# Kernel tuning notes

Measured on AMD Instinct MI355X. Metric: run time of the kernel, lower is better.

The kernel has to match this reference:

```python
import jax, jax.numpy as jnp
import numpy as np

B = 1024        # number of graphs in batch
NNODES = 64     # nodes per graph
NODE = 4        # node feature size
EDGEF = 2       # edge feature size
HID = 32        # hidden_dim
NFACT = 3       # num_factories
NE = 1024       # edges per graph (self.edges list length)


def setup_inputs() -> dict:
    key = jax.random.key(0)
    ks = jax.random.split(key, 12)
    rng = np.random.default_rng(1)
    # per-graph edge list (self.edges in the torch module)
    edges = rng.integers(0, NNODES, size=(NE, 2))
    edges_src = jnp.asarray(edges[:, 0], dtype=jnp.int32)   # [NE]
    edges_dst = jnp.asarray(edges[:, 1], dtype=jnp.int32)   # [NE]
    # batched edge_index for EdgeConv: same per-graph edges offset by b*NNODES
    offs = np.arange(B, dtype=np.int64)[:, None] * NNODES   # [B,1]
    ei_src = (edges[:, 0][None, :] + offs).reshape(-1)
    ei_dst = (edges[:, 1][None, :] + offs).reshape(-1)
    edge_index = jnp.asarray(np.stack([ei_src, ei_dst], 0), dtype=jnp.int32)  # [2, B*NE]

    N = B * NNODES
    E = B * NE
    x = jax.random.normal(ks[0], (N, NODE), dtype=jnp.float32)
    edge_attr = jax.random.normal(ks[1], (E, EDGEF), dtype=jnp.float32)
    action = jax.random.uniform(ks[2], (B, NE + NFACT), dtype=jnp.float32)

    s = 0.1
    W1 = jax.random.normal(ks[3], (2 * NODE + EDGEF, HID), dtype=jnp.float32) * s
    b1 = jnp.zeros((HID,), jnp.float32)
    W2 = jax.random.normal(ks[4], (HID, HID), dtype=jnp.float32) * s
    b2 = jnp.zeros((HID,), jnp.float32)
    D = (NODE + HID) * 2 + 1  # 73
    Wl = jax.random.normal(ks[5], (D, HID), dtype=jnp.float32) * s
    bl = jnp.zeros((HID,), jnp.float32)
    Wv = jax.random.normal(ks[6], (HID, 1), dtype=jnp.float32) * s
    bv = jnp.zeros((1,), jnp.float32)

    return {"x": x, "edge_index": edge_index, "edge_attr": edge_attr,
            "action": action, "edges_src": edges_src, "edges_dst": edges_dst,
            "W1": W1, "b1": b1, "W2": W2, "b2": b2,
            "Wl": Wl, "bl": bl, "Wv": Wv, "bv": bv}


def reference(x, edge_index, edge_attr, action, edges_src, edges_dst,
              W1, b1, W2, b2, Wl, bl, Wv, bv):
    N = x.shape[0]
    src = edge_index[0]  # flow='target_to_source': x_i = x[src], aggregate at src
    dst = edge_index[1]
    # EdgeConv message: MLP(cat[x_i, x_j, edge_attr])
    tmp = jnp.concatenate([x[src], x[dst], edge_attr], axis=1)  # [E, 10]
    msg = jax.nn.relu(tmp @ W1 + b1) @ W2 + b2                  # [E, HID]
    x_pp = jax.ops.segment_sum(msg, src, num_segments=N)        # scatter-add
    # concat node feats with conv output, split into graphs
    h = jnp.concatenate([x, x_pp], axis=1).reshape(B, NNODES, NODE + HID)  # [B,NN,36]
    # gather per-edge endpoint features
    ef = jnp.concatenate([h[:, edges_src], h[:, edges_dst]], axis=2)       # [B,NE,72]
    # factory features: last NFACT nodes duplicated
    pf = jnp.concatenate([h[:, -NFACT:], h[:, -NFACT:]], axis=-1)          # [B,NF,72]
    feats = jnp.concatenate([ef, pf], axis=1)                               # [B,NE+NF,72]
    concat = jnp.concatenate([feats, action[..., None]], axis=-1)           # [B,NE+NF,73]
    hidden = jax.nn.relu(concat @ Wl + bl)                                  # [B,NE+NF,HID]
    v = hidden @ Wv + bv                                                    # [B,NE+NF,1]
    return jnp.sum(v, axis=1).squeeze(-1)                                   # [B]
```

## Files before the change

kernel.cpp:

```cpp
#include <hip/hip_runtime.h>

#define NNODES 64
#define HID 32
#define NFACT 3
#define NE 1024
#define NROWS (NE + NFACT)
#define TPB 256
#define STR 36
#define QSTRH 20
#define MAXTILES 128
#define EPT (NE / TPB)

typedef short bf16x8 __attribute__((ext_vector_type(8)));
typedef float f32x4  __attribute__((ext_vector_type(4)));
typedef float f32x16 __attribute__((ext_vector_type(16)));

__device__ __forceinline__ unsigned pack_bf2(float lo, float hi) {
    unsigned ul = __builtin_bit_cast(unsigned, lo);
    unsigned uh = __builtin_bit_cast(unsigned, hi);
    ul += 0x7fffu + ((ul >> 16) & 1u);
    uh += 0x7fffu + ((uh >> 16) & 1u);
    return (ul >> 16) | (uh & 0xffff0000u);
}
__device__ __forceinline__ short f2bf(float f) {
    unsigned u = __builtin_bit_cast(unsigned, f);
    u += 0x7fffu + ((u >> 16) & 1u);
    return (short)(u >> 16);
}
__device__ __forceinline__ float bflo(unsigned u) { return __builtin_bit_cast(float, u << 16); }
__device__ __forceinline__ float bfhi(unsigned u) { return __builtin_bit_cast(float, u & 0xffff0000u); }
__device__ __forceinline__ float4 fma4(float a, float4 w, float4 c) {
    c.x = fmaf(a, w.x, c.x); c.y = fmaf(a, w.y, c.y);
    c.z = fmaf(a, w.z, c.z); c.w = fmaf(a, w.w, c.w);
    return c;
}

__global__ __launch_bounds__(TPB, 4) void critic_fused(
    const float* __restrict__ x,
    const float* __restrict__ edge_attr,
    const float* __restrict__ action,
    const int*   __restrict__ es,
    const int*   __restrict__ ed,
    const float* __restrict__ W1,
    const float* __restrict__ b1,
    const float* __restrict__ W2,
    const float* __restrict__ b2,
    const float* __restrict__ Wl,
    const float* __restrict__ bl,
    const float* __restrict__ Wv,
    const float* __restrict__ bv,
    float* __restrict__ out)
{
    const int b    = blockIdx.x;
    const int tid  = threadIdx.x;
    const int lane = tid & 63;
    const int wv   = tid >> 6;
    const int quad = lane >> 4;
    const int m16  = lane & 15;
    const int kh   = quad * 8;

    __shared__ __align__(16) float4 xs4[NNODES];
    __shared__ __align__(16) float  xpp[NNODES * STR];
    __shared__ __align__(16) float  qp0[NNODES * STR];
    __shared__ __align__(16) float  qp1[NNODES * STR];
    __shared__ __align__(16) float  W1s[10 * HID];
    __shared__ float  b1s[HID];
    __shared__ float  wred[TPB / 64];
    __shared__ int    sdeg[NNODES], soff[NNODES], scnt[NNODES];
    __shared__ int    tns[MAXTILES];
    __shared__ int    pep[MAXTILES * 16];
    __shared__ int    snt;

    unsigned* qh0 = (unsigned*)qp0;
    unsigned* qh1 = (unsigned*)qp1;

    if (tid < NNODES) { xs4[tid] = ((const float4*)x)[b * NNODES + tid]; sdeg[tid] = 0; scnt[tid] = 0; }
    if (tid < 80) ((float4*)W1s)[tid] = ((const float4*)W1)[tid];
    if (tid < HID) b1s[tid] = b1[tid];
    if (tid < MAXTILES) tns[tid] = 0;
#pragma unroll
    for (int i = 0; i < MAXTILES * 16 / TPB; i++) pep[tid + i * TPB] = 0xFFF;
#pragma unroll 1
    for (int i = tid; i < NNODES * STR; i += TPB) xpp[i] = 0.0f;

    int ces[EPT], ced[EPT];
#pragma unroll
    for (int i = 0; i < EPT; i++) {
        ces[i] = es[tid + i * TPB];
        ced[i] = ed[tid + i * TPB];
    }
    __syncthreads();

#pragma unroll
    for (int i = 0; i < EPT; i++) atomicAdd(&sdeg[ces[i]], 1);
    {
        const int n  = lane;
        const int k0 = wv * 8;
        const float4 xv = xs4[n];
        const float4* b1v = (const float4*)&b1s[k0];
        float4 q1a = b1v[0], q1b = b1v[1];
        float4 q2a = make_float4(0.f, 0.f, 0.f, 0.f), q2b = q2a;
#pragma unroll 1
        for (int i = 0; i < 4; i++) {
            const float xi = (i == 0) ? xv.x : (i == 1) ? xv.y : (i == 2) ? xv.z : xv.w;
            const float4* wa = (const float4*)&W1s[i * HID + k0];
            const float4* wb = (const float4*)&W1s[(4 + i) * HID + k0];
            q1a = fma4(xi, wa[0], q1a); q1b = fma4(xi, wa[1], q1b);
            q2a = fma4(xi, wb[0], q2a); q2b = fma4(xi, wb[1], q2b);
        }
        uint4 p1, p2;
        p1.x = pack_bf2(q1a.x, q1a.y); p1.y = pack_bf2(q1a.z, q1a.w);
        p1.z = pack_bf2(q1b.x, q1b.y); p1.w = pack_bf2(q1b.z, q1b.w);
        p2.x = pack_bf2(q2a.x, q2a.y); p2.y = pack_bf2(q2a.z, q2a.w);
        p2.z = pack_bf2(q2b.x, q2b.y); p2.w = pack_bf2(q2b.z, q2b.w);
        *(uint4*)&qh0[n * QSTRH + wv * 4] = p1;
        *(uint4*)&qh1[n * QSTRH + wv * 4] = p2;
    }
    __syncthreads();

    if (tid < NNODES) {
        const int cnt = (sdeg[tid] + 15) >> 4;
        int scan = cnt;
#pragma unroll
        for (int o = 1; o < 64; o <<= 1) {
            const int v = __shfl_up(scan, o);
            if (tid >= o) scan += v;
        }
        const int base = scan - cnt;
        soff[tid] = base;
        if (tid == NNODES - 1) snt = scan;
#pragma unroll 1
        for (int j = 0; j < cnt; j++) tns[base + j] = tid;
    }
    __syncthreads();

#pragma unroll
    for (int i = 0; i < EPT; i++) {
        const int n = ces[i];
        const int idx = atomicAdd(&scnt[n], 1);
        pep[soff[n] * 16 + idx] = (tid + i * TPB) | (ced[i] << 12) | (n << 18);
    }
    __syncthreads();

    {
        const float2* ea2 = (const float2*)edge_attr + (size_t)b * NE;
        const int NW   = TPB / 64;
        const int klo  = (lane >> 5) * 8;
        const int klo2 = klo >> 1;
        const int n32  = lane & 31;

        const float4* w8l = (const float4*)&W1s[8 * HID + klo];
        const float4* w8h = (const float4*)&W1s[8 * HID + 16 + klo];
        const float4* w9l = (const float4*)&W1s[9 * HID + klo];
        const float4* w9h = (const float4*)&W1s[9 * HID + 16 + klo];
        const float4 w8a = w8l[0], w8b = w8l[1], w8c = w8h[0], w8d = w8h[1];
        const float4 w9a = w9l[0], w9b = w9l[1], w9c = w9h[0], w9d = w9h[1];

        bf16x8 bfA, bfB;
#pragma unroll
        for (int j = 0; j < 8; j++) {
            bfA[j] = f2bf(W2[(klo + j) * HID + n32]);
            bfB[j] = f2bf(W2[(16 + klo + j) * HID + n32]);
        }

        const int np = (snt + 1) >> 1;

#pragma unroll 1
        for (int p = wv; p < np; p += NW) {
            const int raw = pep[p * 32 + n32];
            const int tA  = tns[2 * p];
            const int tB  = tns[2 * p + 1];
            const int e    = raw & 0xFFF;
            const bool pad = (e == 0xFFF);
            const int d0   = (raw >> 12) & 63;
            const int nd   = (raw >> 18) & 63;
            const float2 ea = ea2[pad ? 0 : e];

            const uint4 A1 = *(const uint4*)&qh0[nd * QSTRH + klo2];
            const uint4 A2 = *(const uint4*)&qh0[nd * QSTRH + 8 + klo2];
            const uint4 G1 = *(const uint4*)&qh1[d0 * QSTRH + klo2];
            const uint4 G2 = *(const uint4*)&qh1[d0 * QSTRH + 8 + klo2];

            const float hx0 = fmaxf(bflo(A1.x) + bflo(G1.x) + ea.x * w8a.x + ea.y * w9a.x, 0.f);
            const float hx1 = fmaxf(bfhi(A1.x) + bfhi(G1.x) + ea.x * w8a.y + ea.y * w9a.y, 0.f);
            const float hx2 = fmaxf(bflo(A1.y) + bflo(G1.y) + ea.x * w8a.z + ea.y * w9a.z, 0.f);
            const float hx3 = fmaxf(bfhi(A1.y) + bfhi(G1.y) + ea.x * w8a.w + ea.y * w9a.w, 0.f);
            const float hx4 = fmaxf(bflo(A1.z) + bflo(G1.z) + ea.x * w8b.x + ea.y * w9b.x, 0.f);
            const float hx5 = fmaxf(bfhi(A1.z) + bfhi(G1.z) + ea.x * w8b.y + ea.y * w9b.y, 0.f);
            const float hx6 = fmaxf(bflo(A1.w) + bflo(G1.w) + ea.x * w8b.z + ea.y * w9b.z, 0.f);
            const float hx7 = fmaxf(bfhi(A1.w) + bfhi(G1.w) + ea.x * w8b.w + ea.y * w9b.w, 0.f);
            const float hy0 = fmaxf(bflo(A2.x) + bflo(G2.x) + ea.x * w8c.x + ea.y * w9c.x, 0.f);
            const float hy1 = fmaxf(bfhi(A2.x) + bfhi(G2.x) + ea.x * w8c.y + ea.y * w9c.y, 0.f);
            const float hy2 = fmaxf(bflo(A2.y) + bflo(G2.y) + ea.x * w8c.z + ea.y * w9c.z, 0.f);
            const float hy3 = fmaxf(bfhi(A2.y) + bfhi(G2.y) + ea.x * w8c.w + ea.y * w9c.w, 0.f);
            const float hy4 = fmaxf(bflo(A2.z) + bflo(G2.z) + ea.x * w8d.x + ea.y * w9d.x, 0.f);
            const float hy5 = fmaxf(bfhi(A2.z) + bfhi(G2.z) + ea.x * w8d.y + ea.y * w9d.y, 0.f);
            const float hy6 = fmaxf(bflo(A2.w) + bflo(G2.w) + ea.x * w8d.z + ea.y * w9d.z, 0.f);
            const float hy7 = fmaxf(bfhi(A2.w) + bfhi(G2.w) + ea.x * w8d.w + ea.y * w9d.w, 0.f);

            uint4 pkA, pkB;
            pkA.x = pad ? 0u : pack_bf2(hx0, hx1);
            pkA.y = pad ? 0u : pack_bf2(hx2, hx3);
            pkA.z = pad ? 0u : pack_bf2(hx4, hx5);
            pkA.w = pad ? 0u : pack_bf2(hx6, hx7);
            pkB.x = pad ? 0u : pack_bf2(hy0, hy1);
            pkB.y = pad ? 0u : pack_bf2(hy2, hy3);
            pkB.z = pad ? 0u : pack_bf2(hy4, hy5);
            pkB.w = pad ? 0u : pack_bf2(hy6, hy7);
            const bf16x8 afA = __builtin_bit_cast(bf16x8, pkA);
            const bf16x8 afB = __builtin_bit_cast(bf16x8, pkB);

            f32x16 c;
#pragma unroll
            for (int j = 0; j < 16; j++) c[j] = 0.0f;
            c = __builtin_amdgcn_mfma_f32_32x32x16_bf16(afA, bfA, c, 0, 0, 0);
            c = __builtin_amdgcn_mfma_f32_32x32x16_bf16(afB, bfB, c, 0, 0, 0);

            float sA = ((c[0] + c[1]) + (c[2] + c[3])) + ((c[4] + c[5]) + (c[6] + c[7]));
            float sB = ((c[8] + c[9]) + (c[10] + c[11])) + ((c[12] + c[13]) + (c[14] + c[15]));
            sA += __shfl_xor(sA, 32);
            sB += __shfl_xor(sB, 32);
            const int   nst = (lane < 32) ? tA : tB;
            const float sv  = (lane < 32) ? sA : sB;
            atomicAdd(&xpp[nst * STR + n32], sv);
        }
    }
    __syncthreads();

    bf16x8 bP1a, bP1b, bP2a, bP2b;
#pragma unroll
    for (int j = 0; j < 8; j++) {
        bP1a[j] = f2bf(Wl[(4 + kh + j) * HID + m16]);
        bP1b[j] = f2bf(Wl[(4 + kh + j) * HID + 16 + m16]);
        bP2a[j] = f2bf(Wl[(40 + kh + j) * HID + m16]);
        bP2b[j] = f2bf(Wl[(40 + kh + j) * HID + 16 + m16]);
    }
    float wx1a[4], wx1b[4], wx2a[4], wx2b[4];
#pragma unroll
    for (int i = 0; i < 4; i++) {
        wx1a[i] = Wl[i * HID + m16];
        wx1b[i] = Wl[i * HID + 16 + m16];
        wx2a[i] = Wl[(36 + i) * HID + m16];
        wx2b[i] = Wl[(36 + i) * HID + 16 + m16];
    }
    const float blca = bl[m16], blcb = bl[16 + m16];
    float b2k[8];
#pragma unroll
    for (int j = 0; j < 8; j++) b2k[j] = b2[kh + j];
    const int   mrow = wv * 16 + m16;
    const float dn   = (float)sdeg[mrow];

    {
        const float4* xr = (const float4*)&xpp[mrow * STR + kh];
        float4 x0 = xr[0], x1 = xr[1];
        x0.x = fmaf(dn, b2k[0], x0.x); x0.y = fmaf(dn, b2k[1], x0.y);
        x0.z = fmaf(dn, b2k[2], x0.z); x0.w = fmaf(dn, b2k[3], x0.w);
        x1.x = fmaf(dn, b2k[4], x1.x); x1.y = fmaf(dn, b2k[5], x1.y);
        x1.z = fmaf(dn, b2k[6], x1.z); x1.w = fmaf(dn, b2k[7], x1.w);
        uint4 packed;
        packed.x = pack_bf2(x0.x, x0.y);
        packed.y = pack_bf2(x0.z, x0.w);
        packed.z = pack_bf2(x1.x, x1.y);
        packed.w = pack_bf2(x1.z, x1.w);
        const bf16x8 af = __builtin_bit_cast(bf16x8, packed);

        f32x4 c1a, c1b, c2a, c2b;
#pragma unroll
        for (int r = 0; r < 4; r++) {
            const float4 xv = xs4[wv * 16 + quad * 4 + r];
            float a0 = blca, a1 = blcb, a2 = 0.f, a3 = 0.f;
#pragma unroll
            for (int i = 0; i < 4; i++) {
                const float xi = (i == 0) ? xv.x : (i == 1) ? xv.y : (i == 2) ? xv.z : xv.w;
                a0 = fmaf(xi, wx1a[i], a0);
                a1 = fmaf(xi, wx1b[i], a1);
                a2 = fmaf(xi, wx2a[i], a2);
                a3 = fmaf(xi, wx2b[i], a3);
            }
            c1a[r] = a0; c1b[r] = a1; c2a[r] = a2; c2b[r] = a3;
        }
        c1a = __builtin_amdgcn_mfma_f32_16x16x32_bf16(af, bP1a, c1a, 0, 0, 0);
        c1b = __builtin_amdgcn_mfma_f32_16x16x32_bf16(af, bP1b, c1b, 0, 0, 0);
        c2a = __builtin_amdgcn_mfma_f32_16x16x32_bf16(af, bP2a, c2a, 0, 0, 0);
        c2b = __builtin_amdgcn_mfma_f32_16x16x32_bf16(af, bP2b, c2b, 0, 0, 0);

        __syncthreads();
#pragma unroll
        for (int r = 0; r < 4; r++) {
            const int row = wv * 16 + quad * 4 + r;
            qp0[row * STR + m16]      = c1a[r];
            qp0[row * STR + 16 + m16] = c1b[r];
            qp1[row * STR + m16]      = c2a[r];
            qp1[row * STR + 16 + m16] = c2b[r];
        }
    }
    __syncthreads();

    float vsum = 0.0f;
    {
        const float* actb = action + (size_t)b * NROWS;
        const float bvv = bv[0];
        const float* Wl72 = Wl + 72 * HID;
#pragma unroll 1
        for (int i = 0; i < 4; i++) {
            const int na = ces[i], nb = ced[i];
            const float a = actb[tid + i * TPB];
            const float4* p1v = (const float4*)&qp0[na * STR];
            const float4* p2v = (const float4*)&qp1[nb * STR];
            float v0 = bvv, v1 = 0.0f;
#pragma unroll 1
            for (int q = 0; q < 8; q += 2) {
                const float4 pa0 = p1v[q],     pb0 = p2v[q];
                const float4 pa1 = p1v[q + 1], pb1 = p2v[q + 1];
                const int k = q * 4;
                v0 += fmaxf(pa0.x + pb0.x + a * Wl72[k+0], 0.f) * Wv[k+0];
                v1 += fmaxf(pa0.y + pb0.y + a * Wl72[k+1], 0.f) * Wv[k+1];
                v0 += fmaxf(pa0.z + pb0.z + a * Wl72[k+2], 0.f) * Wv[k+2];
                v1 += fmaxf(pa0.w + pb0.w + a * Wl72[k+3], 0.f) * Wv[k+3];
                v0 += fmaxf(pa1.x + pb1.x + a * Wl72[k+4], 0.f) * Wv[k+4];
                v1 += fmaxf(pa1.y + pb1.y + a * Wl72[k+5], 0.f) * Wv[k+5];
                v0 += fmaxf(pa1.z + pb1.z + a * Wl72[k+6], 0.f) * Wv[k+6];
                v1 += fmaxf(pa1.w + pb1.w + a * Wl72[k+7], 0.f) * Wv[k+7];
            }
            vsum += v0 + v1;
        }
        if (tid < NFACT) {
            const int r = NE + tid;
            const int na = NNODES - NFACT + tid;
            const float a = actb[r];
            const float4* p1v = (const float4*)&qp0[na * STR];
            const float4* p2v = (const float4*)&qp1[na * STR];
            float v = bvv;
#pragma unroll 1
            for (int q = 0; q < 8; q++) {
                const float4 pa = p1v[q], pb = p2v[q];
                const int k = q * 4;
                v += fmaxf(pa.x + pb.x + a * Wl72[k+0], 0.f) * Wv[k+0];
                v += fmaxf(pa.y + pb.y + a * Wl72[k+1], 0.f) * Wv[k+1];
                v += fmaxf(pa.z + pb.z + a * Wl72[k+2], 0.f) * Wv[k+2];
                v += fmaxf(pa.w + pb.w + a * Wl72[k+3], 0.f) * Wv[k+3];
            }
            vsum += v;
        }
    }

#pragma unroll
    for (int off = 32; off > 0; off >>= 1)
        vsum += __shfl_down(vsum, off, 64);
    if ((tid & 63) == 0) wred[tid >> 6] = vsum;
    __syncthreads();
    if (tid == 0) {
        float t = 0.0f;
#pragma unroll
        for (int w = 0; w < TPB / 64; w++) t += wred[w];
        out[b] = t;
    }
}

extern "C" void kernel_launch(void* const* d_in, const int* in_sizes, int n_in,
                              void* d_out, int out_size, void* d_ws, size_t ws_size,
                              hipStream_t stream) {
    const float* x         = (const float*)d_in[0];
    const float* edge_attr = (const float*)d_in[2];
    const float* action    = (const float*)d_in[3];
    const int*   es        = (const int*)d_in[4];
    const int*   ed        = (const int*)d_in[5];
    const float* W1        = (const float*)d_in[6];
    const float* b1        = (const float*)d_in[7];
    const float* W2        = (const float*)d_in[8];
    const float* b2        = (const float*)d_in[9];
    const float* Wl        = (const float*)d_in[10];
    const float* bl        = (const float*)d_in[11];
    const float* Wv        = (const float*)d_in[12];
    const float* bv        = (const float*)d_in[13];
    float* out = (float*)d_out;

    critic_fused<<<dim3(out_size), dim3(TPB), 0, stream>>>(
        x, edge_attr, action, es, ed, W1, b1, W2, b2, Wl, bl, Wv, bv, out);
}
```

Before: 125.1 us.

## Double block size to 512 threads and split per-node projections across wave groups

Raises threads per block from 256 to 512 and sets launch bounds to 8 waves per SIMD occupancy hint. The first-layer node projections and the Wl projection MFMAs are split so waves 0-3 compute the source half and waves 4-7 the destination half, instead of each wave doing both. The xpp zeroing is vectorised to float4 stores. This shortens per-thread serial work and adds parallelism per graph, at the cost of more register pressure and barrier cost across more waves. Hidden sections such as the edge tile loop and the final reduction depend on TPB/EPT, and their correctness is not visible.

```diff
diff --git a/kernel.cpp b/kernel.cpp
--- a/kernel.cpp
+++ b/kernel.cpp
@@ -5,7 +5,7 @@
 #define NFACT 3
 #define NE 1024
 #define NROWS (NE + NFACT)
-#define TPB 256
+#define TPB 512
 #define STR 36
 #define QSTRH 20
 #define MAXTILES 128
@@ -35,7 +35,7 @@
     return c;
 }
 
-__global__ __launch_bounds__(TPB, 4) void critic_fused(
+__global__ __launch_bounds__(TPB, 8) void critic_fused(
     const float* __restrict__ x,
     const float* __restrict__ edge_attr,
     const float* __restrict__ action,
@@ -80,8 +80,11 @@
     if (tid < MAXTILES) tns[tid] = 0;
 #pragma unroll
     for (int i = 0; i < MAXTILES * 16 / TPB; i++) pep[tid + i * TPB] = 0xFFF;
-#pragma unroll 1
-    for (int i = tid; i < NNODES * STR; i += TPB) xpp[i] = 0.0f;
+    {
+        const float4 z4 = make_float4(0.f, 0.f, 0.f, 0.f);
+#pragma unroll 1
+        for (int i = tid; i < NNODES * STR / 4; i += TPB) ((float4*)xpp)[i] = z4;
+    }
 
     int ces[EPT], ced[EPT];
 #pragma unroll
@@ -94,27 +97,29 @@
 #pragma unroll
     for (int i = 0; i < EPT; i++) atomicAdd(&sdeg[ces[i]], 1);
     {
-        const int n  = lane;
-        const int k0 = wv * 8;
+        const int  n  = lane;
+        const int  k0 = (wv & 3) * 8;
+        const bool g1 = (wv < 4);
+        const int  rb = g1 ? 0 : 4;
         const float4 xv = xs4[n];
-        const float4* b1v = (const float4*)&b1s[k0];
-        float4 q1a = b1v[0], q1b = b1v[1];
-        float4 q2a = make_float4(0.f, 0.f, 0.f, 0.f), q2b = q2a;
+        float4 qa, qb;
+        if (g1) {
+            const float4* b1v = (const float4*)&b1s[k0];
+            qa = b1v[0]; qb = b1v[1];
+        } else {
+            qa = make_float4(0.f, 0.f, 0.f, 0.f); qb = qa;
+        }
 #pragma unroll 1
         for (int i = 0; i < 4; i++) {
             const float xi = (i == 0) ? xv.x : (i == 1) ? xv.y : (i == 2) ? xv.z : xv.w;
-            const float4* wa = (const float4*)&W1s[i * HID + k0];
-            const float4* wb = (const float4*)&W1s[(4 + i) * HID + k0];
-            q1a = fma4(xi, wa[0], q1a); q1b = fma4(xi, wa[1], q1b);
-            q2a = fma4(xi, wb[0], q2a); q2b = fma4(xi, wb[1], q2b);
-        }
-        uint4 p1, p2;
-        p1.x = pack_bf2(q1a.x, q1a.y); p1.y = pack_bf2(q1a.z, q1a.w);
-        p1.z = pack_bf2(q1b.x, q1b.y); p1.w = pack_bf2(q1b.z, q1b.w);
-        p2.x = pack_bf2(q2a.x, q2a.y); p2.y = pack_bf2(q2a.z, q2a.w);
-        p2.z = pack_bf2(q2b.x, q2b.y); p2.w = pack_bf2(q2b.z, q2b.w);
-        *(uint4*)&qh0[n * QSTRH + wv * 4] = p1;
-        *(uint4*)&qh1[n * QSTRH + wv * 4] = p2;
+            const float4* wa = (const float4*)&W1s[(rb + i) * HID + k0];
+            qa = fma4(xi, wa[0], qa); qb = fma4(xi, wa[1], qb);
+        }
+        uint4 p;
+        p.x = pack_bf2(qa.x, qa.y); p.y = pack_bf2(qa.z, qa.w);
+        p.z = pack_bf2(qb.x, qb.y); p.w = pack_bf2(qb.z, qb.w);
+        unsigned* dst = g1 ? qh0 : qh1;
+        *(uint4*)&dst[n * QSTRH + (wv & 3) * 4] = p;
     }
     __syncthreads();
 
@@ -227,27 +232,27 @@
     }
     __syncthreads();
 
-    bf16x8 bP1a, bP1b, bP2a, bP2b;
+    const bool g1p   = (wv < 4);
+    const int  cbase = g1p ? 4 : 40;
+    const int  xbase = g1p ? 0 : 36;
+    bf16x8 bPa, bPb;
 #pragma unroll
     for (int j = 0; j < 8; j++) {
-        bP1a[j] = f2bf(Wl[(4 + kh + j) * HID + m16]);
-        bP1b[j] = f2bf(Wl[(4 + kh + j) * HID + 16 + m16]);
-        bP2a[j] = f2bf(Wl[(40 + kh + j) * HID + m16]);
-        bP2b[j] = f2bf(Wl[(40 + kh + j) * HID + 16 + m16]);
-    }
-    float wx1a[4], wx1b[4], wx2a[4], wx2b[4];
+        bPa[j] = f2bf(Wl[(cbase + kh + j) * HID + m16]);
+        bPb[j] = f2bf(Wl[(cbase + kh + j) * HID + 16 + m16]);
+    }
+    float wxa[4], wxb[4];
 #pragma unroll
     for (int i = 0; i < 4; i++) {
-        wx1a[i] = Wl[i * HID + m16];
-        wx1b[i] = Wl[i * HID + 16 + m16];
-        wx2a[i] = Wl[(36 + i) * HID + m16];
-        wx2b[i] = Wl[(36 + i) * HID + 16 + m16];
-    }
-    const float blca = bl[m16], blcb = bl[16 + m16];
+        wxa[i] = Wl[(xbase + i) * HID + m16];
+        wxb[i] = Wl[(xbase + i) * HID + 16 + m16];
+    }
+    const float bca = g1p ? bl[m16] : 0.f;
+    const float bcb = g1p ? bl[16 + m16] : 0.f;
     float b2k[8];
 #pragma unroll
     for (int j = 0; j < 8; j++) b2k[j] = b2[kh + j];
-    const int   mrow = wv * 16 + m16;
+    const int   mrow = (wv & 3) * 16 + m16;
     const float dn   = (float)sdeg[mrow];
 
     {
@@ -264,34 +269,29 @@
         packed.w = pack_bf2(x1.z, x1.w);
         const bf16x8 af = __builtin_bit_cast(bf16x8, packed);
 
-        f32x4 c1a, c1b, c2a, c2b;
+        f32x4 ca, cb;
 #pragma unroll
         for (int r = 0; r < 4; r++) {
-            const float4 xv = xs4[wv * 16 + quad * 4 + r];
-            float a0 = blca, a1 = blcb, a2 = 0.f, a3 = 0.f;
+            const float4 xv = xs4[(wv & 3) * 16 + quad * 4 + r];
+            float a0 = bca, a1 = bcb;
 #pragma unroll
             for (int i = 0; i < 4; i++) {
                 const float xi = (i == 0) ? xv.x : (i == 1) ? xv.y : (i == 2) ? xv.z : xv.w;
-                a0 = fmaf(xi, wx1a[i], a0);
-                a1 = fmaf(xi, wx1b[i], a1);
-                a2 = fmaf(xi, wx2a[i], a2);
-                a3 = fmaf(xi, wx2b[i], a3);
+                a0 = fmaf(xi, wxa[i], a0);
+                a1 = fmaf(xi, wxb[i], a1);
             }
-            c1a[r] = a0; c1b[r] = a1; c2a[r] = a2; c2b[r] = a3;
-        }
-        c1a = __builtin_amdgcn_mfma_f32_16x16x32_bf16(af, bP1a, c1a, 0, 0, 0);
-        c1b = __builtin_amdgcn_mfma_f32_16x16x32_bf16(af, bP1b, c1b, 0, 0, 0);
-        c2a = __builtin_amdgcn_mfma_f32_16x16x32_bf16(af, bP2a, c2a, 0, 0, 0);
-        c2b = __builtin_amdgcn_mfma_f32_16x16x32_bf16(af, bP2b, c2b, 0, 0, 0);
+            ca[r] = a0; cb[r] = a1;
+        }
+        ca = __builtin_amdgcn_mfma_f32_16x16x32_bf16(af, bPa, ca, 0, 0, 0);
+        cb = __builtin_amdgcn_mfma_f32_16x16x32_bf16(af, bPb, cb, 0, 0, 0);
 
         __syncthreads();
+        float* dst = g1p ? qp0 : qp1;
 #pragma unroll
         for (int r = 0; r < 4; r++) {
-            const int row = wv * 16 + quad * 4 + r;
-            qp0[row * STR + m16]      = c1a[r];
-            qp0[row * STR + 16 + m16] = c1b[r];
-            qp1[row * STR + m16]      = c2a[r];
-            qp1[row * STR + 16 + m16] = c2b[r];
+            const int row = (wv & 3) * 16 + quad * 4 + r;
+            dst[row * STR + m16]      = ca[r];
+            dst[row * STR + 16 + m16] = cb[r];
         }
     }
     __syncthreads();
@@ -302,7 +302,7 @@
         const float bvv = bv[0];
         const float* Wl72 = Wl + 72 * HID;
 #pragma unroll 1
-        for (int i = 0; i < 4; i++) {
+        for (int i = 0; i < EPT; i++) {
             const int na = ces[i], nb = ced[i];
             const float a = actb[tid + i * TPB];
             const float4* p1v = (const float4*)&qp0[na * STR];
```

New measurement: 139.9 us. 11.9% more time.
